# Kernel tuning notes

Measured on AMD Instinct MI355X. Metric: run time of the kernel, lower is better.

The kernel has to match this reference:

```python
import jax, jax.numpy as jnp
import numpy as np

N_GROUP = 8
N_ITER = 3


def setup_inputs() -> dict:
    key = jax.random.key(0)
    k1, k2 = jax.random.split(key)
    B, H, W, C = 32, 28, 28, 512          # C = n_group * p = 8 * 64
    g, p, fo = N_GROUP, C // N_GROUP, 256  # per-group in-channels p, out filters fo
    x = jax.random.normal(k1, (B, H, W, C), dtype=jnp.float32)
    # per-group 1x1 conv blocks; he_normal-style scale over fan_in = p
    kernels = jax.random.normal(k2, (g, p, fo), dtype=jnp.float32) * np.float32(np.sqrt(2.0 / p))
    bias = jnp.zeros((fo,), dtype=jnp.float32)
    return {"x": x, "kernels": kernels, "bias": bias}


def reference(x, kernels, bias):
    # x: [B,H,W,g*p], kernels: [g,p,fo], bias: [fo]
    B, H, W, C = x.shape
    g, p, fo = kernels.shape
    # Grouped 1x1 conv == block-diagonal dense conv in the original (zero pads
    # kill all cross-group terms), expressed directly as a grouped contraction.
    xg = x.reshape(B, H, W, g, p)
    con = jnp.einsum('bhwgp,gpf->bhwgf', xg, kernels)  # [B,H,W,g,fo]
    # Dynamic routing over the group axis.
    beta = jnp.zeros((), dtype=con.dtype)
    out = None
    for i in range(N_ITER):
        alpha = jax.nn.sigmoid(beta)                         # scalar, then [B,H,W,g,1]
        v = jnp.sum(con * alpha, axis=-2, keepdims=True)     # [B,H,W,1,fo]
        if i == N_ITER - 1:
            out = v[..., 0, :] + bias                        # [B,H,W,fo]
        else:
            beta = beta + jnp.sum(con * v, axis=-1, keepdims=True)  # [B,H,W,g,1]
    return out


if __name__ == '__main__':
    inp = setup_inputs()
    y = jax.jit(reference)(**inp)
    print(y.shape, y.dtype)
```

## Files before the change

### kernel.cpp

```cpp
#include <hip/hip_runtime.h>
#include <hip/hip_bf16.h>

#define GRP   8
#define PCH   64
#define FO    256
#define CIN   512
#define PTILE 16
#define XROW  520

typedef __attribute__((ext_vector_type(8))) short bf16x8;
typedef __attribute__((ext_vector_type(4))) float f32x4;

__device__ __forceinline__ short f2b(float f) {
    __hip_bfloat16 h = __float2bfloat16(f);
    short s;
    __builtin_memcpy(&s, &h, 2);
    return s;
}
__device__ __forceinline__ float sigmoidf_(float b) {
    return 1.0f / (1.0f + __expf(-b));
}
__device__ __forceinline__ float dot4(f32x4 a, f32x4 b) {
    return fmaf(a[0], b[0], fmaf(a[1], b[1], fmaf(a[2], b[2], a[3] * b[3])));
}

__global__ void repack_w(const float* __restrict__ wk, unsigned short* __restrict__ wpk) {
    int id = blockIdx.x * 256 + threadIdx.x;
    int j    = id & 7;
    int lane = (id >> 3) & 63;
    int kb   = (id >> 9) & 1;
    int t    = (id >> 10) & 15;
    int g    = id >> 14;
    int p = kb * 32 + (lane >> 4) * 8 + j;
    int f = t * 16 + (lane & 15);
    unsigned short u;
    __hip_bfloat16 h = __float2bfloat16(wk[(g * PCH + p) * FO + f]);
    __builtin_memcpy(&u, &h, 2);
    wpk[id] = u;
}

__global__ __launch_bounds__(1024, 1)
void dynroute_reg(const float* __restrict__ x, const unsigned short* __restrict__ wpk,
                  const float* __restrict__ bias, float* __restrict__ out) {
    __shared__ unsigned short xs[PTILE * XROW];
    __shared__ float part_s[16][PTILE][8];
    __shared__ float alpha1_s[PTILE][8];
    __shared__ float alpha2_s[PTILE][8];

    const int tid  = threadIdx.x;
    const int lane = tid & 63;
    const int wave = tid >> 6;
    const int pos  = lane & 15;
    const int lq   = lane >> 4;
    const long m0  = (long)blockIdx.x * PTILE;

    {
        const int srow = wave;
        const int scol = (lane) * 8;
        const float* xp = x + (m0 + srow) * CIN + scol;
        const float4 u0 = *reinterpret_cast<const float4*>(xp);
        const float4 u1 = *reinterpret_cast<const float4*>(xp + 4);
        bf16x8 v;
        v[0] = f2b(u0.x); v[1] = f2b(u0.y); v[2] = f2b(u0.z); v[3] = f2b(u0.w);
        v[4] = f2b(u1.x); v[5] = f2b(u1.y); v[6] = f2b(u1.z); v[7] = f2b(u1.w);
        *reinterpret_cast<bf16x8*>(&xs[srow * XROW + scol]) = v;
    }
    __syncthreads();

    f32x4 acc[GRP];
    {
        const unsigned short* xrow = &xs[pos * XROW];
        #pragma unroll
        for (int g = 0; g < GRP; ++g) {
            const bf16x8 xf0 = *reinterpret_cast<const bf16x8*>(&xrow[g * 64 + lq * 8]);
            const bf16x8 xf1 = *reinterpret_cast<const bf16x8*>(&xrow[g * 64 + 32 + lq * 8]);
            const bf16x8 wf0 = *reinterpret_cast<const bf16x8*>(
                wpk + ((((g * 16 + wave) * 2 + 0) * 64 + lane) << 3));
            const bf16x8 wf1 = *reinterpret_cast<const bf16x8*>(
                wpk + ((((g * 16 + wave) * 2 + 1) * 64 + lane) << 3));
            f32x4 a = {0.f, 0.f, 0.f, 0.f};
            a = __builtin_amdgcn_mfma_f32_16x16x32_bf16(wf0, xf0, a, 0, 0, 0);
            a = __builtin_amdgcn_mfma_f32_16x16x32_bf16(wf1, xf1, a, 0, 0, 0);
            acc[g] = a;
        }
    }

    f32x4 s0 = acc[0];
    #pragma unroll
    for (int g = 1; g < GRP; ++g) s0 += acc[g];

    float d1[GRP];
    #pragma unroll
    for (int g = 0; g < GRP; ++g) d1[g] = dot4(acc[g], s0);
    #pragma unroll
    for (int g = 0; g < GRP; ++g) {
        d1[g] += __shfl_xor(d1[g], 16, 64);
        d1[g] += __shfl_xor(d1[g], 32, 64);
    }
    if (lq == 0) {
        float4 v0 = {d1[0], d1[1], d1[2], d1[3]};
        float4 v1 = {d1[4], d1[5], d1[6], d1[7]};
        *reinterpret_cast<float4*>(&part_s[wave][pos][0]) = v0;
        *reinterpret_cast<float4*>(&part_s[wave][pos][4]) = v1;
    }
    __syncthreads();

    float b1r = 0.f;
    if (tid < 128) {
        const int rp = tid >> 3, rg = tid & 7;
        float s = 0.f;
        #pragma unroll
        for (int w = 0; w < 16; ++w) s += part_s[w][rp][rg];
        b1r = 0.5f * s;
        alpha1_s[rp][rg] = sigmoidf_(b1r);
    }
    __syncthreads();

    float a1v[GRP];
    #pragma unroll
    for (int g = 0; g < GRP; ++g) a1v[g] = alpha1_s[pos][g];
    f32x4 sa0 = acc[0] * a1v[0];
    #pragma unroll
    for (int g = 1; g < GRP; ++g) sa0 = a1v[g] * acc[g] + sa0;

    float d2[GRP];
    #pragma unroll
    for (int g = 0; g < GRP; ++g) d2[g] = dot4(acc[g], sa0);
    #pragma unroll
    for (int g = 0; g < GRP; ++g) {
        d2[g] += __shfl_xor(d2[g], 16, 64);
        d2[g] += __shfl_xor(d2[g], 32, 64);
    }
    if (lq == 0) {
        float4 v0 = {d2[0], d2[1], d2[2], d2[3]};
        float4 v1 = {d2[4], d2[5], d2[6], d2[7]};
        *reinterpret_cast<float4*>(&part_s[wave][pos][0]) = v0;
        *reinterpret_cast<float4*>(&part_s[wave][pos][4]) = v1;
    }
    __syncthreads();

    if (tid < 128) {
        const int rp = tid >> 3, rg = tid & 7;
        float s = 0.f;
        #pragma unroll
        for (int w = 0; w < 16; ++w) s += part_s[w][rp][rg];
        alpha2_s[rp][rg] = sigmoidf_(b1r + s);
    }
    __syncthreads();

    float a2v[GRP];
    #pragma unroll
    for (int g = 0; g < GRP; ++g) a2v[g] = alpha2_s[pos][g];
    const float4 bb = *reinterpret_cast<const float4*>(bias + wave * 16 + lq * 4);
    f32x4 o0 = {bb.x, bb.y, bb.z, bb.w};
    #pragma unroll
    for (int g = 0; g < GRP; ++g) o0 = a2v[g] * acc[g] + o0;

    *reinterpret_cast<float4*>(out + (m0 + pos) * FO + wave * 16 + lq * 4) =
        *reinterpret_cast<float4*>(&o0);
}

extern "C" void kernel_launch(void* const* d_in, const int* in_sizes, int n_in,
                              void* d_out, int out_size, void* d_ws, size_t ws_size,
                              hipStream_t stream) {
    const float* x    = (const float*)d_in[0];
    const float* wk   = (const float*)d_in[1];
    const float* bias = (const float*)d_in[2];
    float* out        = (float*)d_out;
    unsigned short* wpk = (unsigned short*)d_ws;

    hipLaunchKernelGGL(repack_w, dim3(512), dim3(256), 0, stream, wk, wpk);

    const int M = in_sizes[0] / CIN;
    hipLaunchKernelGGL(dynroute_reg, dim3(M / PTILE), dim3(1024), 0, stream,
                       x, wpk, bias, out);
}
```

Baseline: 51.03 us.

## Make routing kernel persistent with double-buffered x prefetch and Gram-matrix routing

Replaces the one-tile-per-block launch with 224 persistent blocks that each process 7 tiles, double-buffering x in LDS and prefetching the next tile into registers while the MFMAs run. Both routing iterations are computed algebraically from a per-position 8x8 symmetric Gram matrix (36 dot products), so one cross-wave reduction replaces two. The aim is to overlap global loads with compute and cut the number of barrier/reduction rounds. In exchange it uses more registers for 36 partials, adds shuffle traffic, leaves the 16-thread alpha solve serial, and hardcodes the tile count to the test shape.

New measurement: 126.8 us. 2.48x slower.

```diff
diff --git a/kernel.cpp b/kernel.cpp
--- a/kernel.cpp
+++ b/kernel.cpp
@@ -7,6 +7,9 @@
 #define CIN   512
 #define PTILE 16
 #define XROW  520
+#define TPB   7
+#define NTILE 1568
+#define NBLK  224
 
 typedef __attribute__((ext_vector_type(8))) short bf16x8;
 typedef __attribute__((ext_vector_type(4))) float f32x4;
@@ -22,6 +25,10 @@
 }
 __device__ __forceinline__ float dot4(f32x4 a, f32x4 b) {
     return fmaf(a[0], b[0], fmaf(a[1], b[1], fmaf(a[2], b[2], a[3] * b[3])));
+}
+__device__ __forceinline__ constexpr int TRI(int i, int j) {
+    int a = i < j ? i : j, b = i < j ? j : i;
+    return a * 8 - a * (a - 1) / 2 + (b - a);
 }
 
 __global__ void repack_w(const float* __restrict__ wk, unsigned short* __restrict__ wpk) {
@@ -40,124 +47,148 @@
 }
 
 __global__ __launch_bounds__(1024, 1)
-void dynroute_reg(const float* __restrict__ x, const unsigned short* __restrict__ wpk,
-                  const float* __restrict__ bias, float* __restrict__ out) {
-    __shared__ unsigned short xs[PTILE * XROW];
-    __shared__ float part_s[16][PTILE][8];
-    __shared__ float alpha1_s[PTILE][8];
-    __shared__ float alpha2_s[PTILE][8];
+void dynroute_pers(const float* __restrict__ x, const unsigned short* __restrict__ wpk,
+                   const float* __restrict__ bias, float* __restrict__ out) {
+    __shared__ unsigned short xs[2][PTILE * XROW];
+    __shared__ float part_s[16 * PTILE * 36];
+    __shared__ float Gs[PTILE * 36];
+    __shared__ float alpha_s[PTILE][8];
 
     const int tid  = threadIdx.x;
     const int lane = tid & 63;
     const int wave = tid >> 6;
     const int pos  = lane & 15;
     const int lq   = lane >> 4;
-    const long m0  = (long)blockIdx.x * PTILE;
+
+    const int t0 = blockIdx.x * TPB;
+
+    const float4 bb = *reinterpret_cast<const float4*>(bias + wave * 16 + lq * 4);
 
     {
-        const int srow = wave;
-        const int scol = (lane) * 8;
-        const float* xp = x + (m0 + srow) * CIN + scol;
-        const float4 u0 = *reinterpret_cast<const float4*>(xp);
-        const float4 u1 = *reinterpret_cast<const float4*>(xp + 4);
+        const float* p = x + ((size_t)(t0 * PTILE + wave)) * CIN + lane * 8;
+        const float4 r0 = *reinterpret_cast<const float4*>(p);
+        const float4 r1 = *reinterpret_cast<const float4*>(p + 4);
         bf16x8 v;
-        v[0] = f2b(u0.x); v[1] = f2b(u0.y); v[2] = f2b(u0.z); v[3] = f2b(u0.w);
-        v[4] = f2b(u1.x); v[5] = f2b(u1.y); v[6] = f2b(u1.z); v[7] = f2b(u1.w);
-        *reinterpret_cast<bf16x8*>(&xs[srow * XROW + scol]) = v;
+        v[0] = f2b(r0.x); v[1] = f2b(r0.y); v[2] = f2b(r0.z); v[3] = f2b(r0.w);
+        v[4] = f2b(r1.x); v[5] = f2b(r1.y); v[6] = f2b(r1.z); v[7] = f2b(r1.w);
+        *reinterpret_cast<bf16x8*>(&xs[0][wave * XROW + lane * 8]) = v;
+    }
+    float4 ra, rb;
+    {
+        const float* p = x + ((size_t)((t0 + 1) * PTILE + wave)) * CIN + lane * 8;
+        ra = *reinterpret_cast<const float4*>(p);
+        rb = *reinterpret_cast<const float4*>(p + 4);
     }
     __syncthreads();
 
-    f32x4 acc[GRP];
-    {
-        const unsigned short* xrow = &xs[pos * XROW];
+    for (int i = 0; i < TPB; ++i) {
+        const int buf  = i & 1;
+        const int tile = t0 + i;
+
+        f32x4 acc[GRP];
+        {
+            const unsigned short* xrow = &xs[buf][pos * XROW];
+            #pragma unroll
+            for (int g = 0; g < GRP; ++g) {
+                const bf16x8 xf0 = *reinterpret_cast<const bf16x8*>(&xrow[g * 64 + lq * 8]);
+                const bf16x8 xf1 = *reinterpret_cast<const bf16x8*>(&xrow[g * 64 + 32 + lq * 8]);
+                const bf16x8 wf0 = *reinterpret_cast<const bf16x8*>(
+                    wpk + ((((g * 16 + wave) * 2 + 0) * 64 + lane) << 3));
+                const bf16x8 wf1 = *reinterpret_cast<const bf16x8*>(
+                    wpk + ((((g * 16 + wave) * 2 + 1) * 64 + lane) << 3));
+                f32x4 a = {0.f, 0.f, 0.f, 0.f};
+                a = __builtin_amdgcn_mfma_f32_16x16x32_bf16(wf0, xf0, a, 0, 0, 0);
+                a = __builtin_amdgcn_mfma_f32_16x16x32_bf16(wf1, xf1, a, 0, 0, 0);
+                acc[g] = a;
+            }
+        }
+
+        {
+            bf16x8 v;
+            v[0] = f2b(ra.x); v[1] = f2b(ra.y); v[2] = f2b(ra.z); v[3] = f2b(ra.w);
+            v[4] = f2b(rb.x); v[5] = f2b(rb.y); v[6] = f2b(rb.z); v[7] = f2b(rb.w);
+            *reinterpret_cast<bf16x8*>(&xs[buf ^ 1][wave * XROW + lane * 8]) = v;
+            int tn = tile + 2;
+            if (tn > NTILE - 1) tn = NTILE - 1;
+            const float* p = x + ((size_t)(tn * PTILE + wave)) * CIN + lane * 8;
+            ra = *reinterpret_cast<const float4*>(p);
+            rb = *reinterpret_cast<const float4*>(p + 4);
+        }
+
+        float pg[36];
+        {
+            int idx = 0;
+            #pragma unroll
+            for (int gi = 0; gi < GRP; ++gi)
+                #pragma unroll
+                for (int gj = gi; gj < GRP; ++gj)
+                    pg[idx++] = dot4(acc[gi], acc[gj]);
+        }
         #pragma unroll
-        for (int g = 0; g < GRP; ++g) {
-            const bf16x8 xf0 = *reinterpret_cast<const bf16x8*>(&xrow[g * 64 + lq * 8]);
-            const bf16x8 xf1 = *reinterpret_cast<const bf16x8*>(&xrow[g * 64 + 32 + lq * 8]);
-            const bf16x8 wf0 = *reinterpret_cast<const bf16x8*>(
-                wpk + ((((g * 16 + wave) * 2 + 0) * 64 + lane) << 3));
-            const bf16x8 wf1 = *reinterpret_cast<const bf16x8*>(
-                wpk + ((((g * 16 + wave) * 2 + 1) * 64 + lane) << 3));
-            f32x4 a = {0.f, 0.f, 0.f, 0.f};
-            a = __builtin_amdgcn_mfma_f32_16x16x32_bf16(wf0, xf0, a, 0, 0, 0);
-            a = __builtin_amdgcn_mfma_f32_16x16x32_bf16(wf1, xf1, a, 0, 0, 0);
-            acc[g] = a;
+        for (int j = 0; j < 36; ++j) {
+            pg[j] += __shfl_xor(pg[j], 16, 64);
+            pg[j] += __shfl_xor(pg[j], 32, 64);
+        }
+        if (lq == 0) {
+            float* dst = &part_s[(wave * PTILE + pos) * 36];
+            #pragma unroll
+            for (int j4 = 0; j4 < 9; ++j4) {
+                float4 w4 = {pg[4 * j4], pg[4 * j4 + 1], pg[4 * j4 + 2], pg[4 * j4 + 3]};
+                *reinterpret_cast<float4*>(dst + 4 * j4) = w4;
+            }
+        }
+        __syncthreads();
+
+        if (tid < 576) {
+            const int pp = tid / 36;
+            const int j  = tid - pp * 36;
+            float s0 = 0.f, s1 = 0.f, s2 = 0.f, s3 = 0.f;
+            #pragma unroll
+            for (int w = 0; w < 16; w += 4) {
+                s0 += part_s[((w + 0) * PTILE + pp) * 36 + j];
+                s1 += part_s[((w + 1) * PTILE + pp) * 36 + j];
+                s2 += part_s[((w + 2) * PTILE + pp) * 36 + j];
+                s3 += part_s[((w + 3) * PTILE + pp) * 36 + j];
+            }
+            Gs[pp * 36 + j] = (s0 + s1) + (s2 + s3);
+        }
+        __syncthreads();
+
+        if (tid < 16) {
+            float g36[36];
+            #pragma unroll
+            for (int j = 0; j < 36; ++j) g36[j] = Gs[tid * 36 + j];
+            float b1[8], a1[8];
+            #pragma unroll
+            for (int g = 0; g < 8; ++g) {
+                float s = 0.f;
+                #pragma unroll
+                for (int g2 = 0; g2 < 8; ++g2) s += g36[TRI(g, g2)];
+                b1[g] = 0.5f * s;
+                a1[g] = sigmoidf_(b1[g]);
+            }
+            #pragma unroll
+            for (int g = 0; g < 8; ++g) {
+                float s = b1[g];
+                #pragma unroll
+                for (int g2 = 0; g2 < 8; ++g2) s = fmaf(g36[TRI(g, g2)], a1[g2], s);
+                alpha_s[tid][g] = sigmoidf_(s);
+            }
+        }
+        __syncthreads();
+
+        {
+            const float4 A0 = *reinterpret_cast<const float4*>(&alpha_s[pos][0]);
+            const float4 A1 = *reinterpret_cast<const float4*>(&alpha_s[pos][4]);
+            const float av[8] = {A0.x, A0.y, A0.z, A0.w, A1.x, A1.y, A1.z, A1.w};
+            f32x4 o = {bb.x, bb.y, bb.z, bb.w};
+            #pragma unroll
+            for (int g = 0; g < GRP; ++g) o = av[g] * acc[g] + o;
+            *reinterpret_cast<float4*>(
+                out + ((size_t)(tile * PTILE + pos)) * FO + wave * 16 + lq * 4) =
+                *reinterpret_cast<float4*>(&o);
         }
     }
-
-    f32x4 s0 = acc[0];
-    #pragma unroll
-    for (int g = 1; g < GRP; ++g) s0 += acc[g];
-
-    float d1[GRP];
-    #pragma unroll
-    for (int g = 0; g < GRP; ++g) d1[g] = dot4(acc[g], s0);
-    #pragma unroll
-    for (int g = 0; g < GRP; ++g) {
-        d1[g] += __shfl_xor(d1[g], 16, 64);
-        d1[g] += __shfl_xor(d1[g], 32, 64);
-    }
-    if (lq == 0) {
-        float4 v0 = {d1[0], d1[1], d1[2], d1[3]};
-        float4 v1 = {d1[4], d1[5], d1[6], d1[7]};
-        *reinterpret_cast<float4*>(&part_s[wave][pos][0]) = v0;
-        *reinterpret_cast<float4*>(&part_s[wave][pos][4]) = v1;
-    }
-    __syncthreads();
-
-    float b1r = 0.f;
-    if (tid < 128) {
-        const int rp = tid >> 3, rg = tid & 7;
-        float s = 0.f;
-        #pragma unroll
-        for (int w = 0; w < 16; ++w) s += part_s[w][rp][rg];
-        b1r = 0.5f * s;
-        alpha1_s[rp][rg] = sigmoidf_(b1r);
-    }
-    __syncthreads();
-
-    float a1v[GRP];
-    #pragma unroll
-    for (int g = 0; g < GRP; ++g) a1v[g] = alpha1_s[pos][g];
-    f32x4 sa0 = acc[0] * a1v[0];
-    #pragma unroll
-    for (int g = 1; g < GRP; ++g) sa0 = a1v[g] * acc[g] + sa0;
-
-    float d2[GRP];
-    #pragma unroll
-    for (int g = 0; g < GRP; ++g) d2[g] = dot4(acc[g], sa0);
-    #pragma unroll
-    for (int g = 0; g < GRP; ++g) {
-        d2[g] += __shfl_xor(d2[g], 16, 64);
-        d2[g] += __shfl_xor(d2[g], 32, 64);
-    }
-    if (lq == 0) {
-        float4 v0 = {d2[0], d2[1], d2[2], d2[3]};
-        float4 v1 = {d2[4], d2[5], d2[6], d2[7]};
-        *reinterpret_cast<float4*>(&part_s[wave][pos][0]) = v0;
-        *reinterpret_cast<float4*>(&part_s[wave][pos][4]) = v1;
-    }
-    __syncthreads();
-
-    if (tid < 128) {
-        const int rp = tid >> 3, rg = tid & 7;
-        float s = 0.f;
-        #pragma unroll
-        for (int w = 0; w < 16; ++w) s += part_s[w][rp][rg];
-        alpha2_s[rp][rg] = sigmoidf_(b1r + s);
-    }
-    __syncthreads();
-
-    float a2v[GRP];
-    #pragma unroll
-    for (int g = 0; g < GRP; ++g) a2v[g] = alpha2_s[pos][g];
-    const float4 bb = *reinterpret_cast<const float4*>(bias + wave * 16 + lq * 4);
-    f32x4 o0 = {bb.x, bb.y, bb.z, bb.w};
-    #pragma unroll
-    for (int g = 0; g < GRP; ++g) o0 = a2v[g] * acc[g] + o0;
-
-    *reinterpret_cast<float4*>(out + (m0 + pos) * FO + wave * 16 + lq * 4) =
-        *reinterpret_cast<float4*>(&o0);
 }
 
 extern "C" void kernel_launch(void* const* d_in, const int* in_sizes, int n_in,
@@ -170,8 +201,6 @@
     unsigned short* wpk = (unsigned short*)d_ws;
 
     hipLaunchKernelGGL(repack_w, dim3(512), dim3(256), 0, stream, wk, wpk);
-
-    const int M = in_sizes[0] / CIN;
-    hipLaunchKernelGGL(dynroute_reg, dim3(M / PTILE), dim3(1024), 0, stream,
+    hipLaunchKernelGGL(dynroute_pers, dim3(NBLK), dim3(1024), 0, stream,
                        x, wpk, bias, out);
 }
```

## Make routing kernel persistent with double-buffered register prefetch of x tiles

Applied to the files above, without the earlier changes.

Replaces the one-tile-per-block grid with a persistent grid of 256 blocks, each looping over 6 or 7 tiles of 16 positions. The next tile's x rows are prefetched into registers and written to a second LDS buffer while the current tile is processed, so global load latency overlaps the MFMA and routing work. This also amortizes launch and setup overhead across tiles. The tile count and grid size are hardcoded to this input shape, and a 256-block grid may underfill the 256 CUs if occupancy is limited to one 1024-thread block per CU.

After: 87.96 us. 1.72x slower.

```diff
diff --git a/kernel.cpp b/kernel.cpp
--- a/kernel.cpp
+++ b/kernel.cpp
@@ -7,6 +7,8 @@
 #define CIN   512
 #define PTILE 16
 #define XROW  520
+#define NTILE 1568
+#define GRIDB 256
 
 typedef __attribute__((ext_vector_type(8))) short bf16x8;
 typedef __attribute__((ext_vector_type(4))) float f32x4;
@@ -40,9 +42,9 @@
 }
 
 __global__ __launch_bounds__(1024, 1)
-void dynroute_reg(const float* __restrict__ x, const unsigned short* __restrict__ wpk,
-                  const float* __restrict__ bias, float* __restrict__ out) {
-    __shared__ unsigned short xs[PTILE * XROW];
+void dynroute_pers(const float* __restrict__ x, const unsigned short* __restrict__ wpk,
+                   const float* __restrict__ bias, float* __restrict__ out) {
+    __shared__ unsigned short xs[2][PTILE * XROW];
     __shared__ float part_s[16][PTILE][8];
     __shared__ float alpha1_s[PTILE][8];
     __shared__ float alpha2_s[PTILE][8];
@@ -52,112 +54,139 @@
     const int wave = tid >> 6;
     const int pos  = lane & 15;
     const int lq   = lane >> 4;
-    const long m0  = (long)blockIdx.x * PTILE;
+    const int bid  = blockIdx.x;
+    const int niter = (bid < NTILE - 6 * GRIDB) ? 7 : 6;
+
+    const float4 bb = *reinterpret_cast<const float4*>(bias + wave * 16 + lq * 4);
 
     {
-        const int srow = wave;
-        const int scol = (lane) * 8;
-        const float* xp = x + (m0 + srow) * CIN + scol;
-        const float4 u0 = *reinterpret_cast<const float4*>(xp);
-        const float4 u1 = *reinterpret_cast<const float4*>(xp + 4);
+        const float* p = x + ((size_t)(bid * PTILE + wave)) * CIN + lane * 8;
+        const float4 r0 = *reinterpret_cast<const float4*>(p);
+        const float4 r1 = *reinterpret_cast<const float4*>(p + 4);
         bf16x8 v;
-        v[0] = f2b(u0.x); v[1] = f2b(u0.y); v[2] = f2b(u0.z); v[3] = f2b(u0.w);
-        v[4] = f2b(u1.x); v[5] = f2b(u1.y); v[6] = f2b(u1.z); v[7] = f2b(u1.w);
-        *reinterpret_cast<bf16x8*>(&xs[srow * XROW + scol]) = v;
+        v[0] = f2b(r0.x); v[1] = f2b(r0.y); v[2] = f2b(r0.z); v[3] = f2b(r0.w);
+        v[4] = f2b(r1.x); v[5] = f2b(r1.y); v[6] = f2b(r1.z); v[7] = f2b(r1.w);
+        *reinterpret_cast<bf16x8*>(&xs[0][wave * XROW + lane * 8]) = v;
+    }
+    float4 ra, rb;
+    {
+        int tn = bid + GRIDB;
+        if (tn >= NTILE) tn = bid;
+        const float* p = x + ((size_t)(tn * PTILE + wave)) * CIN + lane * 8;
+        ra = *reinterpret_cast<const float4*>(p);
+        rb = *reinterpret_cast<const float4*>(p + 4);
     }
     __syncthreads();
 
-    f32x4 acc[GRP];
-    {
-        const unsigned short* xrow = &xs[pos * XROW];
+    for (int i = 0; i < niter; ++i) {
+        const int tile = bid + i * GRIDB;
+        const int buf  = i & 1;
+
+        f32x4 acc[GRP];
+        {
+            const unsigned short* xrow = &xs[buf][pos * XROW];
+            #pragma unroll
+            for (int g = 0; g < GRP; ++g) {
+                const bf16x8 xf0 = *reinterpret_cast<const bf16x8*>(&xrow[g * 64 + lq * 8]);
+                const bf16x8 xf1 = *reinterpret_cast<const bf16x8*>(&xrow[g * 64 + 32 + lq * 8]);
+                const bf16x8 wf0 = *reinterpret_cast<const bf16x8*>(
+                    wpk + ((((g * 16 + wave) * 2 + 0) * 64 + lane) << 3));
+                const bf16x8 wf1 = *reinterpret_cast<const bf16x8*>(
+                    wpk + ((((g * 16 + wave) * 2 + 1) * 64 + lane) << 3));
+                f32x4 a = {0.f, 0.f, 0.f, 0.f};
+                a = __builtin_amdgcn_mfma_f32_16x16x32_bf16(wf0, xf0, a, 0, 0, 0);
+                a = __builtin_amdgcn_mfma_f32_16x16x32_bf16(wf1, xf1, a, 0, 0, 0);
+                acc[g] = a;
+            }
+        }
+
+        {
+            bf16x8 v;
+            v[0] = f2b(ra.x); v[1] = f2b(ra.y); v[2] = f2b(ra.z); v[3] = f2b(ra.w);
+            v[4] = f2b(rb.x); v[5] = f2b(rb.y); v[6] = f2b(rb.z); v[7] = f2b(rb.w);
+            *reinterpret_cast<bf16x8*>(&xs[buf ^ 1][wave * XROW + lane * 8]) = v;
+            int tn = tile + 2 * GRIDB;
+            if (tn >= NTILE) tn = tile;
+            const float* p = x + ((size_t)(tn * PTILE + wave)) * CIN + lane * 8;
+            ra = *reinterpret_cast<const float4*>(p);
+            rb = *reinterpret_cast<const float4*>(p + 4);
+        }
+
+        f32x4 s0 = acc[0];
+        #pragma unroll
+        for (int g = 1; g < GRP; ++g) s0 += acc[g];
+
+        float d1[GRP];
+        #pragma unroll
+        for (int g = 0; g < GRP; ++g) d1[g] = dot4(acc[g], s0);
         #pragma unroll
         for (int g = 0; g < GRP; ++g) {
-            const bf16x8 xf0 = *reinterpret_cast<const bf16x8*>(&xrow[g * 64 + lq * 8]);
-            const bf16x8 xf1 = *reinterpret_cast<const bf16x8*>(&xrow[g * 64 + 32 + lq * 8]);
-            const bf16x8 wf0 = *reinterpret_cast<const bf16x8*>(
-                wpk + ((((g * 16 + wave) * 2 + 0) * 64 + lane) << 3));
-            const bf16x8 wf1 = *reinterpret_cast<const bf16x8*>(
-                wpk + ((((g * 16 + wave) * 2 + 1) * 64 + lane) << 3));
-            f32x4 a = {0.f, 0.f, 0.f, 0.f};
-            a = __builtin_amdgcn_mfma_f32_16x16x32_bf16(wf0, xf0, a, 0, 0, 0);
-            a = __builtin_amdgcn_mfma_f32_16x16x32_bf16(wf1, xf1, a, 0, 0, 0);
-            acc[g] = a;
+            d1[g] += __shfl_xor(d1[g], 16, 64);
+            d1[g] += __shfl_xor(d1[g], 32, 64);
+        }
+        if (lq == 0) {
+            float4 v0 = {d1[0], d1[1], d1[2], d1[3]};
+            float4 v1 = {d1[4], d1[5], d1[6], d1[7]};
+            *reinterpret_cast<float4*>(&part_s[wave][pos][0]) = v0;
+            *reinterpret_cast<float4*>(&part_s[wave][pos][4]) = v1;
+        }
+        __syncthreads();
+
+        float b1r = 0.f;
+        if (tid < 128) {
+            const int rp = tid >> 3, rg = tid & 7;
+            float s = 0.f;
+            #pragma unroll
+            for (int w = 0; w < 16; ++w) s += part_s[w][rp][rg];
+            b1r = 0.5f * s;
+            alpha1_s[rp][rg] = sigmoidf_(b1r);
+        }
+        __syncthreads();
+
+        float a1v[GRP];
+        #pragma unroll
+        for (int g = 0; g < GRP; ++g) a1v[g] = alpha1_s[pos][g];
+        f32x4 sa0 = acc[0] * a1v[0];
+        #pragma unroll
+        for (int g = 1; g < GRP; ++g) sa0 = a1v[g] * acc[g] + sa0;
+
+        float d2[GRP];
+        #pragma unroll
+        for (int g = 0; g < GRP; ++g) d2[g] = dot4(acc[g], sa0);
+        #pragma unroll
+        for (int g = 0; g < GRP; ++g) {
+            d2[g] += __shfl_xor(d2[g], 16, 64);
+            d2[g] += __shfl_xor(d2[g], 32, 64);
+        }
+        if (lq == 0) {
+            float4 v0 = {d2[0], d2[1], d2[2], d2[3]};
+            float4 v1 = {d2[4], d2[5], d2[6], d2[7]};
+            *reinterpret_cast<float4*>(&part_s[wave][pos][0]) = v0;
+            *reinterpret_cast<float4*>(&part_s[wave][pos][4]) = v1;
+        }
+        __syncthreads();
+
+        if (tid < 128) {
+            const int rp = tid >> 3, rg = tid & 7;
+            float s = 0.f;
+            #pragma unroll
+            for (int w = 0; w < 16; ++w) s += part_s[w][rp][rg];
+            alpha2_s[rp][rg] = sigmoidf_(b1r + s);
+        }
+        __syncthreads();
+
+        {
+            const float4 A0 = *reinterpret_cast<const float4*>(&alpha2_s[pos][0]);
+            const float4 A1 = *reinterpret_cast<const float4*>(&alpha2_s[pos][4]);
+            const float av[8] = {A0.x, A0.y, A0.z, A0.w, A1.x, A1.y, A1.z, A1.w};
+            f32x4 o = {bb.x, bb.y, bb.z, bb.w};
+            #pragma unroll
+            for (int g = 0; g < GRP; ++g) o = av[g] * acc[g] + o;
+            *reinterpret_cast<float4*>(
+                out + ((size_t)(tile * PTILE + pos)) * FO + wave * 16 + lq * 4) =
+                *reinterpret_cast<float4*>(&o);
         }
     }
-
-    f32x4 s0 = acc[0];
-    #pragma unroll
-    for (int g = 1; g < GRP; ++g) s0 += acc[g];
-
-    float d1[GRP];
-    #pragma unroll
-    for (int g = 0; g < GRP; ++g) d1[g] = dot4(acc[g], s0);
-    #pragma unroll
-    for (int g = 0; g < GRP; ++g) {
-        d1[g] += __shfl_xor(d1[g], 16, 64);
-        d1[g] += __shfl_xor(d1[g], 32, 64);
-    }
-    if (lq == 0) {
-        float4 v0 = {d1[0], d1[1], d1[2], d1[3]};
-        float4 v1 = {d1[4], d1[5], d1[6], d1[7]};
-        *reinterpret_cast<float4*>(&part_s[wave][pos][0]) = v0;
-        *reinterpret_cast<float4*>(&part_s[wave][pos][4]) = v1;
-    }
-    __syncthreads();
-
-    float b1r = 0.f;
-    if (tid < 128) {
-        const int rp = tid >> 3, rg = tid & 7;
-        float s = 0.f;
-        #pragma unroll
-        for (int w = 0; w < 16; ++w) s += part_s[w][rp][rg];
-        b1r = 0.5f * s;
-        alpha1_s[rp][rg] = sigmoidf_(b1r);
-    }
-    __syncthreads();
-
-    float a1v[GRP];
-    #pragma unroll
-    for (int g = 0; g < GRP; ++g) a1v[g] = alpha1_s[pos][g];
-    f32x4 sa0 = acc[0] * a1v[0];
-    #pragma unroll
-    for (int g = 1; g < GRP; ++g) sa0 = a1v[g] * acc[g] + sa0;
-
-    float d2[GRP];
-    #pragma unroll
-    for (int g = 0; g < GRP; ++g) d2[g] = dot4(acc[g], sa0);
-    #pragma unroll
-    for (int g = 0; g < GRP; ++g) {
-        d2[g] += __shfl_xor(d2[g], 16, 64);
-        d2[g] += __shfl_xor(d2[g], 32, 64);
-    }
-    if (lq == 0) {
-        float4 v0 = {d2[0], d2[1], d2[2], d2[3]};
-        float4 v1 = {d2[4], d2[5], d2[6], d2[7]};
-        *reinterpret_cast<float4*>(&part_s[wave][pos][0]) = v0;
-        *reinterpret_cast<float4*>(&part_s[wave][pos][4]) = v1;
-    }
-    __syncthreads();
-
-    if (tid < 128) {
-        const int rp = tid >> 3, rg = tid & 7;
-        float s = 0.f;
-        #pragma unroll
-        for (int w = 0; w < 16; ++w) s += part_s[w][rp][rg];
-        alpha2_s[rp][rg] = sigmoidf_(b1r + s);
-    }
-    __syncthreads();
-
-    float a2v[GRP];
-    #pragma unroll
-    for (int g = 0; g < GRP; ++g) a2v[g] = alpha2_s[pos][g];
-    const float4 bb = *reinterpret_cast<const float4*>(bias + wave * 16 + lq * 4);
-    f32x4 o0 = {bb.x, bb.y, bb.z, bb.w};
-    #pragma unroll
-    for (int g = 0; g < GRP; ++g) o0 = a2v[g] * acc[g] + o0;
-
-    *reinterpret_cast<float4*>(out + (m0 + pos) * FO + wave * 16 + lq * 4) =
-        *reinterpret_cast<float4*>(&o0);
 }
 
 extern "C" void kernel_launch(void* const* d_in, const int* in_sizes, int n_in,
@@ -170,8 +199,6 @@
     unsigned short* wpk = (unsigned short*)d_ws;
 
     hipLaunchKernelGGL(repack_w, dim3(512), dim3(256), 0, stream, wk, wpk);
-
-    const int M = in_sizes[0] / CIN;
-    hipLaunchKernelGGL(dynroute_reg, dim3(M / PTILE), dim3(1024), 0, stream,
+    hipLaunchKernelGGL(dynroute_pers, dim3(GRIDB), dim3(1024), 0, stream,
                        x, wpk, bias, out);
 }
```

## Halve block size, give each wave two output tiles, keep con packed as bf16

Applied to the files above, without the earlier changes.

The fused routing kernel now runs with 512 threads per block, and each wave computes two 16-column output tiles instead of one. To hold twice the per-thread conv results without spilling, the MFMA outputs are rounded and packed into bf16 pairs in registers and unpacked for each routing dot product and weighted sum. The x staging load is widened to 16 floats per thread, the bf16 conversion is replaced with a manual round-to-nearest-even, and the grid size is hardcoded. This trades precision of the intermediate con values and extra unpack ALU work for smaller blocks and fewer cross-wave partial reductions.

Result: slower. 55.09 us (+8.0%).

```diff
diff --git a/kernel.cpp b/kernel.cpp
--- a/kernel.cpp
+++ b/kernel.cpp
@@ -1,27 +1,27 @@
 #include <hip/hip_runtime.h>
-#include <hip/hip_bf16.h>
 
 #define GRP   8
-#define PCH   64
 #define FO    256
 #define CIN   512
 #define PTILE 16
 #define XROW  520
+#define NTILE 1568
 
 typedef __attribute__((ext_vector_type(8))) short bf16x8;
 typedef __attribute__((ext_vector_type(4))) float f32x4;
 
-__device__ __forceinline__ short f2b(float f) {
-    __hip_bfloat16 h = __float2bfloat16(f);
-    short s;
-    __builtin_memcpy(&s, &h, 2);
-    return s;
-}
+__device__ __forceinline__ unsigned f2bu(float f) {
+    unsigned u = __float_as_uint(f);
+    return (u + 0x7FFFu + ((u >> 16) & 1u)) >> 16;
+}
+__device__ __forceinline__ short f2b(float f) { return (short)f2bu(f); }
+__device__ __forceinline__ unsigned pk2(float a, float b) {
+    return f2bu(a) | (f2bu(b) << 16);
+}
+__device__ __forceinline__ float ulo(unsigned u) { return __uint_as_float(u << 16); }
+__device__ __forceinline__ float uhi(unsigned u) { return __uint_as_float(u & 0xffff0000u); }
 __device__ __forceinline__ float sigmoidf_(float b) {
     return 1.0f / (1.0f + __expf(-b));
-}
-__device__ __forceinline__ float dot4(f32x4 a, f32x4 b) {
-    return fmaf(a[0], b[0], fmaf(a[1], b[1], fmaf(a[2], b[2], a[3] * b[3])));
 }
 
 __global__ void repack_w(const float* __restrict__ wk, unsigned short* __restrict__ wpk) {
@@ -33,17 +33,14 @@
     int g    = id >> 14;
     int p = kb * 32 + (lane >> 4) * 8 + j;
     int f = t * 16 + (lane & 15);
-    unsigned short u;
-    __hip_bfloat16 h = __float2bfloat16(wk[(g * PCH + p) * FO + f]);
-    __builtin_memcpy(&u, &h, 2);
-    wpk[id] = u;
-}
-
-__global__ __launch_bounds__(1024, 1)
-void dynroute_reg(const float* __restrict__ x, const unsigned short* __restrict__ wpk,
-                  const float* __restrict__ bias, float* __restrict__ out) {
+    wpk[id] = (unsigned short)f2bu(wk[(g * 64 + p) * FO + f]);
+}
+
+__global__ __launch_bounds__(512, 1)
+void dynroute_pk(const float* __restrict__ x, const unsigned short* __restrict__ wpk,
+                 const float* __restrict__ bias, float* __restrict__ out) {
     __shared__ unsigned short xs[PTILE * XROW];
-    __shared__ float part_s[16][PTILE][8];
+    __shared__ float part_s[8][PTILE][8];
     __shared__ float alpha1_s[PTILE][8];
     __shared__ float alpha2_s[PTILE][8];
 
@@ -55,43 +52,61 @@
     const long m0  = (long)blockIdx.x * PTILE;
 
     {
-        const int srow = wave;
-        const int scol = (lane) * 8;
-        const float* xp = x + (m0 + srow) * CIN + scol;
-        const float4 u0 = *reinterpret_cast<const float4*>(xp);
-        const float4 u1 = *reinterpret_cast<const float4*>(xp + 4);
-        bf16x8 v;
-        v[0] = f2b(u0.x); v[1] = f2b(u0.y); v[2] = f2b(u0.z); v[3] = f2b(u0.w);
-        v[4] = f2b(u1.x); v[5] = f2b(u1.y); v[6] = f2b(u1.z); v[7] = f2b(u1.w);
-        *reinterpret_cast<bf16x8*>(&xs[srow * XROW + scol]) = v;
-    }
-    __syncthreads();
-
-    f32x4 acc[GRP];
+        const int row = tid >> 5;
+        const int c0  = (tid & 31) * 16;
+        const float* p = x + (m0 + row) * CIN + c0;
+        const float4 u0 = *reinterpret_cast<const float4*>(p);
+        const float4 u1 = *reinterpret_cast<const float4*>(p + 4);
+        const float4 u2 = *reinterpret_cast<const float4*>(p + 8);
+        const float4 u3 = *reinterpret_cast<const float4*>(p + 12);
+        bf16x8 v0, v1;
+        v0[0] = f2b(u0.x); v0[1] = f2b(u0.y); v0[2] = f2b(u0.z); v0[3] = f2b(u0.w);
+        v0[4] = f2b(u1.x); v0[5] = f2b(u1.y); v0[6] = f2b(u1.z); v0[7] = f2b(u1.w);
+        v1[0] = f2b(u2.x); v1[1] = f2b(u2.y); v1[2] = f2b(u2.z); v1[3] = f2b(u2.w);
+        v1[4] = f2b(u3.x); v1[5] = f2b(u3.y); v1[6] = f2b(u3.z); v1[7] = f2b(u3.w);
+        *reinterpret_cast<bf16x8*>(&xs[row * XROW + c0]) = v0;
+        *reinterpret_cast<bf16x8*>(&xs[row * XROW + c0 + 8]) = v1;
+    }
+    __syncthreads();
+
+    unsigned cl[2][GRP], ch[2][GRP];
+    f32x4 S0 = {0.f, 0.f, 0.f, 0.f}, S1 = {0.f, 0.f, 0.f, 0.f};
     {
         const unsigned short* xrow = &xs[pos * XROW];
+        const unsigned short* wb = wpk + wave * 2048 + lane * 8;
         #pragma unroll
         for (int g = 0; g < GRP; ++g) {
             const bf16x8 xf0 = *reinterpret_cast<const bf16x8*>(&xrow[g * 64 + lq * 8]);
             const bf16x8 xf1 = *reinterpret_cast<const bf16x8*>(&xrow[g * 64 + 32 + lq * 8]);
-            const bf16x8 wf0 = *reinterpret_cast<const bf16x8*>(
-                wpk + ((((g * 16 + wave) * 2 + 0) * 64 + lane) << 3));
-            const bf16x8 wf1 = *reinterpret_cast<const bf16x8*>(
-                wpk + ((((g * 16 + wave) * 2 + 1) * 64 + lane) << 3));
-            f32x4 a = {0.f, 0.f, 0.f, 0.f};
-            a = __builtin_amdgcn_mfma_f32_16x16x32_bf16(wf0, xf0, a, 0, 0, 0);
-            a = __builtin_amdgcn_mfma_f32_16x16x32_bf16(wf1, xf1, a, 0, 0, 0);
-            acc[g] = a;
+            #pragma unroll
+            for (int tt = 0; tt < 2; ++tt) {
+                const bf16x8 wf0 = *reinterpret_cast<const bf16x8*>(
+                    wb + g * 16384 + tt * 1024);
+                const bf16x8 wf1 = *reinterpret_cast<const bf16x8*>(
+                    wb + g * 16384 + tt * 1024 + 512);
+                f32x4 a = {0.f, 0.f, 0.f, 0.f};
+                a = __builtin_amdgcn_mfma_f32_16x16x32_bf16(wf0, xf0, a, 0, 0, 0);
+                a = __builtin_amdgcn_mfma_f32_16x16x32_bf16(wf1, xf1, a, 0, 0, 0);
+                if (tt == 0) S0 += a; else S1 += a;
+                cl[tt][g] = pk2(a[0], a[1]);
+                ch[tt][g] = pk2(a[2], a[3]);
+            }
         }
     }
 
-    f32x4 s0 = acc[0];
-    #pragma unroll
-    for (int g = 1; g < GRP; ++g) s0 += acc[g];
-
     float d1[GRP];
     #pragma unroll
-    for (int g = 0; g < GRP; ++g) d1[g] = dot4(acc[g], s0);
+    for (int g = 0; g < GRP; ++g) {
+        float s =      ulo(cl[0][g]) * S0[0];
+        s = fmaf(uhi(cl[0][g]), S0[1], s);
+        s = fmaf(ulo(ch[0][g]), S0[2], s);
+        s = fmaf(uhi(ch[0][g]), S0[3], s);
+        s = fmaf(ulo(cl[1][g]), S1[0], s);
+        s = fmaf(uhi(cl[1][g]), S1[1], s);
+        s = fmaf(ulo(ch[1][g]), S1[2], s);
+        s = fmaf(uhi(ch[1][g]), S1[3], s);
+        d1[g] = s;
+    }
     #pragma unroll
     for (int g = 0; g < GRP; ++g) {
         d1[g] += __shfl_xor(d1[g], 16, 64);
@@ -110,7 +125,7 @@
         const int rp = tid >> 3, rg = tid & 7;
         float s = 0.f;
         #pragma unroll
-        for (int w = 0; w < 16; ++w) s += part_s[w][rp][rg];
+        for (int w = 0; w < 8; ++w) s += part_s[w][rp][rg];
         b1r = 0.5f * s;
         alpha1_s[rp][rg] = sigmoidf_(b1r);
     }
@@ -119,13 +134,31 @@
     float a1v[GRP];
     #pragma unroll
     for (int g = 0; g < GRP; ++g) a1v[g] = alpha1_s[pos][g];
-    f32x4 sa0 = acc[0] * a1v[0];
-    #pragma unroll
-    for (int g = 1; g < GRP; ++g) sa0 = a1v[g] * acc[g] + sa0;
-
+    f32x4 sa0 = {0.f, 0.f, 0.f, 0.f}, sa1 = {0.f, 0.f, 0.f, 0.f};
+    #pragma unroll
+    for (int g = 0; g < GRP; ++g) {
+        sa0[0] = fmaf(a1v[g], ulo(cl[0][g]), sa0[0]);
+        sa0[1] = fmaf(a1v[g], uhi(cl[0][g]), sa0[1]);
+        sa0[2] = fmaf(a1v[g], ulo(ch[0][g]), sa0[2]);
+        sa0[3] = fmaf(a1v[g], uhi(ch[0][g]), sa0[3]);
+        sa1[0] = fmaf(a1v[g], ulo(cl[1][g]), sa1[0]);
+        sa1[1] = fmaf(a1v[g], uhi(cl[1][g]), sa1[1]);
+        sa1[2] = fmaf(a1v[g], ulo(ch[1][g]), sa1[2]);
+        sa1[3] = fmaf(a1v[g], uhi(ch[1][g]), sa1[3]);
+    }
     float d2[GRP];
     #pragma unroll
-    for (int g = 0; g < GRP; ++g) d2[g] = dot4(acc[g], sa0);
+    for (int g = 0; g < GRP; ++g) {
+        float s =      ulo(cl[0][g]) * sa0[0];
+        s = fmaf(uhi(cl[0][g]), sa0[1], s);
+        s = fmaf(ulo(ch[0][g]), sa0[2], s);
+        s = fmaf(uhi(ch[0][g]), sa0[3], s);
+        s = fmaf(ulo(cl[1][g]), sa1[0], s);
+        s = fmaf(uhi(cl[1][g]), sa1[1], s);
+        s = fmaf(ulo(ch[1][g]), sa1[2], s);
+        s = fmaf(uhi(ch[1][g]), sa1[3], s);
+        d2[g] = s;
+    }
     #pragma unroll
     for (int g = 0; g < GRP; ++g) {
         d2[g] += __shfl_xor(d2[g], 16, 64);
@@ -143,7 +176,7 @@
         const int rp = tid >> 3, rg = tid & 7;
         float s = 0.f;
         #pragma unroll
-        for (int w = 0; w < 16; ++w) s += part_s[w][rp][rg];
+        for (int w = 0; w < 8; ++w) s += part_s[w][rp][rg];
         alpha2_s[rp][rg] = sigmoidf_(b1r + s);
     }
     __syncthreads();
@@ -151,13 +184,24 @@
     float a2v[GRP];
     #pragma unroll
     for (int g = 0; g < GRP; ++g) a2v[g] = alpha2_s[pos][g];
-    const float4 bb = *reinterpret_cast<const float4*>(bias + wave * 16 + lq * 4);
-    f32x4 o0 = {bb.x, bb.y, bb.z, bb.w};
-    #pragma unroll
-    for (int g = 0; g < GRP; ++g) o0 = a2v[g] * acc[g] + o0;
-
-    *reinterpret_cast<float4*>(out + (m0 + pos) * FO + wave * 16 + lq * 4) =
-        *reinterpret_cast<float4*>(&o0);
+    const float4 bb0 = *reinterpret_cast<const float4*>(bias + (wave * 2 + 0) * 16 + lq * 4);
+    const float4 bb1 = *reinterpret_cast<const float4*>(bias + (wave * 2 + 1) * 16 + lq * 4);
+    f32x4 o0 = {bb0.x, bb0.y, bb0.z, bb0.w};
+    f32x4 o1 = {bb1.x, bb1.y, bb1.z, bb1.w};
+    #pragma unroll
+    for (int g = 0; g < GRP; ++g) {
+        o0[0] = fmaf(a2v[g], ulo(cl[0][g]), o0[0]);
+        o0[1] = fmaf(a2v[g], uhi(cl[0][g]), o0[1]);
+        o0[2] = fmaf(a2v[g], ulo(ch[0][g]), o0[2]);
+        o0[3] = fmaf(a2v[g], uhi(ch[0][g]), o0[3]);
+        o1[0] = fmaf(a2v[g], ulo(cl[1][g]), o1[0]);
+        o1[1] = fmaf(a2v[g], uhi(cl[1][g]), o1[1]);
+        o1[2] = fmaf(a2v[g], ulo(ch[1][g]), o1[2]);
+        o1[3] = fmaf(a2v[g], uhi(ch[1][g]), o1[3]);
+    }
+    float* ob = out + (m0 + pos) * FO + lq * 4;
+    *reinterpret_cast<float4*>(ob + (wave * 2 + 0) * 16) = *reinterpret_cast<float4*>(&o0);
+    *reinterpret_cast<float4*>(ob + (wave * 2 + 1) * 16) = *reinterpret_cast<float4*>(&o1);
 }
 
 extern "C" void kernel_launch(void* const* d_in, const int* in_sizes, int n_in,
@@ -170,8 +214,6 @@
     unsigned short* wpk = (unsigned short*)d_ws;
 
     hipLaunchKernelGGL(repack_w, dim3(512), dim3(256), 0, stream, wk, wpk);
-
-    const int M = in_sizes[0] / CIN;
-    hipLaunchKernelGGL(dynroute_reg, dim3(M / PTILE), dim3(1024), 0, stream,
+    hipLaunchKernelGGL(dynroute_pk, dim3(NTILE), dim3(512), 0, stream,
                        x, wpk, bias, out);
 }
```
